# Kernel tuning notes

Hardware: AMD Instinct MI355X
Metric: run time of the kernel (lower is better)

Reference implementation:

```python
import jax, jax.numpy as jnp
import numpy as np
from jax import lax

TOTAL_STEPS = 100
BETA_0 = 0.1
BETA_1 = 20.0


def setup_inputs() -> dict:
    key = jax.random.key(0)
    k1, k2 = jax.random.split(key)
    x = jax.random.normal(k1, (64, 256, 64), dtype=jnp.float32)
    noise = jax.random.normal(k2, (TOTAL_STEPS, 64, 256, 64), dtype=jnp.float32)
    return {"x": x, "noise": noise}


def reference(x, noise):
    # VP-SDE Euler-Maruyama forward diffusion, matching forward_sample.
    S = TOTAL_STEPS
    dt = jnp.float32(1.0 / S)
    sqrt_dt = jnp.sqrt(dt)
    # torch loop uses t in [1..S] and computes coefficients at (t-1)/S
    norm_t = (jnp.arange(S, dtype=jnp.float32)) / S  # (t-1)/S for t=1..S

    def step(x_prev, inp):
        nt, n = inp
        beta_t = BETA_0 + nt * (BETA_1 - BETA_0)
        drift = -0.5 * beta_t * x_prev
        x_t = x_prev + drift * dt + jnp.sqrt(beta_t) * n * sqrt_dt
        return x_t, x_t

    _, traj = lax.scan(step, x, (norm_t, noise))  # traj: (S, N, L, D)
    return jnp.concatenate([x[None], traj], axis=0)  # (S+1, N, L, D)
```

## Files before the change

kernel.cpp:

```cpp
#include <hip/hip_runtime.h>
#include <math.h>


#define S_STEPS 100

__global__ __launch_bounds__(256) void vpsde_fwd_kernel(
    const float4* __restrict__ x,
    const float4* __restrict__ noise,
    float4* __restrict__ out,
    int ne4)
{
    __shared__ float s_a[S_STEPS];
    __shared__ float s_b[S_STEPS];

    const int tid = threadIdx.x;
    if (tid < S_STEPS) {
        const float dt      = 1.0f / S_STEPS;
        const float sqrt_dt = 0.1f;
        float nt   = (float)tid * dt;
        float beta = 0.1f + nt * (20.0f - 0.1f);
        s_a[tid] = 1.0f - 0.5f * beta * dt;
        s_b[tid] = sqrtf(beta) * sqrt_dt;
    }
    __syncthreads();

    const int idx = blockIdx.x * blockDim.x + tid;
    if (idx >= ne4) return;

    float4 xv = x[idx];
    out[idx] = xv;

    #pragma unroll 4
    for (int t = 0; t < S_STEPS; ++t) {
        const float a = s_a[t];
        const float b = s_b[t];
        float4 n = noise[(size_t)t * ne4 + idx];
        xv.x = fmaf(a, xv.x, b * n.x);
        xv.y = fmaf(a, xv.y, b * n.y);
        xv.z = fmaf(a, xv.z, b * n.z);
        xv.w = fmaf(a, xv.w, b * n.w);
        out[(size_t)(t + 1) * ne4 + idx] = xv;
    }
}

extern "C" void kernel_launch(void* const* d_in, const int* in_sizes, int n_in,
                              void* d_out, int out_size, void* d_ws, size_t ws_size,
                              hipStream_t stream) {
    const float* x     = (const float*)d_in[0];
    const float* noise = (const float*)d_in[1];
    float* out         = (float*)d_out;

    const int ne  = in_sizes[0];
    const int ne4 = ne / 4;

    const int block = 256;
    const int grid  = (ne4 + block - 1) / block;

    vpsde_fwd_kernel<<<grid, block, 0, stream>>>(
        (const float4*)x, (const float4*)noise, (float4*)out, ne4);
}
```

Baseline: 199.8 us.

## Double-buffer noise loads in windows and use nontemporal loads/stores

```diff
diff --git a/kernel.cpp b/kernel.cpp
--- a/kernel.cpp
+++ b/kernel.cpp
@@ -3,11 +3,15 @@
 
 
 #define S_STEPS 100
+#define U 5
+#define NW (S_STEPS / U)
+
+typedef float f32x4 __attribute__((ext_vector_type(4)));
 
 __global__ __launch_bounds__(256) void vpsde_fwd_kernel(
-    const float4* __restrict__ x,
-    const float4* __restrict__ noise,
-    float4* __restrict__ out,
+    const f32x4* __restrict__ x,
+    const f32x4* __restrict__ noise,
+    f32x4* __restrict__ out,
     int ne4)
 {
     __shared__ float s_a[S_STEPS];
@@ -15,31 +19,47 @@
 
     const int tid = threadIdx.x;
     if (tid < S_STEPS) {
-        const float dt      = 1.0f / S_STEPS;
-        const float sqrt_dt = 0.1f;
-        float nt   = (float)tid * dt;
-        float beta = 0.1f + nt * (20.0f - 0.1f);
+        const float dt = 0.01f;
+        float nt_ = (float)tid * dt;
+        float beta = 0.1f + nt_ * 19.9f;
         s_a[tid] = 1.0f - 0.5f * beta * dt;
-        s_b[tid] = sqrtf(beta) * sqrt_dt;
+        s_b[tid] = sqrtf(beta) * 0.1f;
     }
     __syncthreads();
 
     const int idx = blockIdx.x * blockDim.x + tid;
     if (idx >= ne4) return;
 
-    float4 xv = x[idx];
-    out[idx] = xv;
+    const f32x4* np_ = noise + idx;
+    f32x4* op_ = out + idx;
 
-    #pragma unroll 4
-    for (int t = 0; t < S_STEPS; ++t) {
-        const float a = s_a[t];
-        const float b = s_b[t];
-        float4 n = noise[(size_t)t * ne4 + idx];
-        xv.x = fmaf(a, xv.x, b * n.x);
-        xv.y = fmaf(a, xv.y, b * n.y);
-        xv.z = fmaf(a, xv.z, b * n.z);
-        xv.w = fmaf(a, xv.w, b * n.w);
-        out[(size_t)(t + 1) * ne4 + idx] = xv;
+    f32x4 xv = x[idx];
+    __builtin_nontemporal_store(xv, op_);
+
+    f32x4 A[U], B[U];
+
+    auto loadw = [&](f32x4* buf, int w0) {
+        #pragma unroll
+        for (int k = 0; k < U; ++k)
+            buf[k] = __builtin_nontemporal_load(np_ + (size_t)(w0 + k) * ne4);
+    };
+    auto consume = [&](const f32x4* buf, int w0) {
+        #pragma unroll
+        for (int k = 0; k < U; ++k) {
+            const int t = w0 + k;
+            const float a = s_a[t];
+            const float b = s_b[t];
+            xv = a * xv + b * buf[k];
+            __builtin_nontemporal_store(xv, op_ + (size_t)(t + 1) * ne4);
+        }
+    };
+
+    loadw(A, 0);
+    for (int w = 0; w < NW; w += 2) {
+        loadw(B, (w + 1) * U);
+        consume(A, w * U);
+        if (w + 2 < NW) loadw(A, (w + 2) * U);
+        consume(B, (w + 1) * U);
     }
 }
 
@@ -57,5 +77,5 @@
     const int grid  = (ne4 + block - 1) / block;
 
     vpsde_fwd_kernel<<<grid, block, 0, stream>>>(
-        (const float4*)x, (const float4*)noise, (float4*)out, ne4);
+        (const f32x4*)x, (const f32x4*)noise, (f32x4*)out, ne4);
 }
```

Result: faster. 178.5 us (-10.7%).
